# Kernel optimization log

Measured on AMD Instinct MI355X. Metric: run time of the kernel, lower is better.

Reference implementation:

```python
import jax, jax.numpy as jnp
import numpy as np

N = 10           # node count hardcoded in original module
FEAT_IN = 3      # position(2) + orientation(1)
FEAT_OUT = 16    # 'simple' mode
FEAT_CC = 2 * FEAT_OUT
B = 16384
NEG_SLOPE = 0.2


def _pair_index():
    # Faithful pair ordering: for node i, row 0 is the self-pair (i,i),
    # rows 1..N-1 are j != i in ascending order.
    idx = np.empty((N, N), dtype=np.int32)
    for i in range(N):
        idx[i, 0] = i
        idx[i, 1:] = [j for j in range(N) if j != i]
    return jnp.asarray(idx)


def setup_inputs() -> dict:
    key = jax.random.key(0)
    ks = jax.random.split(key, 12)
    s = 0.1
    return {
        "position": jax.random.normal(ks[0], (B, N, 2), dtype=jnp.float32),
        "orientation": jax.random.normal(ks[1], (B, N, 1), dtype=jnp.float32),
        # preliminary_transform: Linear(3 -> 16)
        "Wp": jax.random.normal(ks[2], (FEAT_IN, FEAT_OUT), dtype=jnp.float32) * s,
        "bp": jax.random.normal(ks[3], (FEAT_OUT,), dtype=jnp.float32) * s,
        # connectivity_net: Linear(32->32), LReLU, Linear(32->8), LReLU, Linear(8->2)
        "W1": jax.random.normal(ks[4], (FEAT_CC, 32), dtype=jnp.float32) * s,
        "b1": jax.random.normal(ks[5], (32,), dtype=jnp.float32) * s,
        "W2": jax.random.normal(ks[6], (32, 8), dtype=jnp.float32) * s,
        "b2": jax.random.normal(ks[7], (8,), dtype=jnp.float32) * s,
        "W3": jax.random.normal(ks[8], (8, 2), dtype=jnp.float32) * s,
        "b3": jax.random.normal(ks[9], (2,), dtype=jnp.float32) * s,
    }


def reference(position, orientation, Wp, bp, W1, b1, W2, b2, W3, b3):
    lrelu = lambda x: jnp.where(x >= 0, x, NEG_SLOPE * x)
    # [B, N, 3] -> [B, N, 16]
    feat = jnp.concatenate([position, orientation], axis=2) @ Wp + bp
    idx = _pair_index()                                   # [N, N]
    vj = feat[:, idx]                                     # [B, N, N, 16] gathered partners
    vi = jnp.broadcast_to(feat[:, :, None, :], vj.shape)  # [B, N, N, 16] source node
    pair = jnp.concatenate([vi, vj], axis=-1)             # [B, N, N, 32]
    h = lrelu(pair @ W1 + b1)
    h = lrelu(h @ W2 + b2)
    big_edge = h @ W3 + b3                                # [B, N, N, 2]
    adjacency = jnp.argmax(big_edge, axis=3)              # [B, N, N]
    return big_edge, adjacency
```

## Files before the change

kernel.cpp:

```cpp
#include <hip/hip_runtime.h>


typedef float v2f __attribute__((ext_vector_type(2)));
typedef float v4f __attribute__((ext_vector_type(4)));

constexpr int G = 12;
constexpr int GB_STRIDE = 36;
constexpr float NEG = 0.2f;

__global__ __launch_bounds__(256, 1) void fuse_kernel(
    const float* __restrict__ Wp, const float* __restrict__ bp,
    const float* __restrict__ W1, const float* __restrict__ b1,
    float* __restrict__ ws)
{
    const int t = threadIdx.x;
    if (t < 192) {
        const int d = t >> 6, k = t & 63;
        const int kk = k & 31;
        const int fo = (k < 32) ? 0 : 16;
        float acc = 0.f;
#pragma unroll
        for (int f = 0; f < 16; ++f)
            acc = fmaf(Wp[d * 16 + f], W1[(fo + f) * 32 + kk], acc);
        ws[d * 64 + k] = acc;
    } else {
        const int k = t - 192;
        const int kk = k & 31;
        const int fo = (k < 32) ? 0 : 16;
        float acc = 0.f;
#pragma unroll
        for (int f = 0; f < 16; ++f)
            acc = fmaf(bp[f], W1[(fo + f) * 32 + kk], acc);
        if (k < 32) acc += b1[k];
        ws[192 + k] = acc;
    }
}

__global__ __launch_bounds__(256, 4) void gpn_kernel(
    const float* __restrict__ pos,
    const float* __restrict__ ori,
    const float* __restrict__ ws,
    const float* __restrict__ W2,
    const float* __restrict__ b2,
    const float* __restrict__ W3,
    const float* __restrict__ b3,
    float* __restrict__ out,
    int B)
{
    __shared__ float sgb[G * 10 * GB_STRIDE];

    const int t = threadIdx.x;
    const int bBase = blockIdx.x * G;
    const int remG = B - bBase;
    const int nLanes = ((remG < G) ? remG : G) * 10 * 2;

    const v4f* m4 = (const v4f*)ws;
    const v4f* c4 = (const v4f*)(ws + 192);

    v4f ga[8];
    const int r = t >> 1;
    const int half = t & 1;
    const int g = r / 10;
    const int i = r - g * 10;
    if (t < nLanes) {
        const int node = bBase * 10 + r;
        const v2f p = ((const v2f*)pos)[node];
        const float o = ori[node];
        v4f* dst = (v4f*)&sgb[r * GB_STRIDE];
#pragma unroll
        for (int q = 0; q < 8; ++q) {
            v4f gg = c4[q];
            gg += p.x * m4[q];
            gg += p.y * m4[16 + q];
            gg += o   * m4[32 + q];
            ga[q] = gg;
        }
#pragma unroll
        for (int qq = 0; qq < 4; ++qq) {
            const int q = 8 + half * 4 + qq;
            v4f gg = c4[q];
            gg += p.x * m4[q];
            gg += p.y * m4[16 + q];
            gg += o   * m4[32 + q];
            dst[q - 8] = gg;
        }
    }
    __syncthreads();

    if (t < nLanes) {
        const v2f* w2p = (const v2f*)W2;
        const v2f* w3p = (const v2f*)W3;
        const v2f bb2_0 = ((const v2f*)b2)[0];
        const v2f bb2_1 = ((const v2f*)b2)[1];
        const v2f bb2_2 = ((const v2f*)b2)[2];
        const v2f bb2_3 = ((const v2f*)b2)[3];
        const v2f bb3   = ((const v2f*)b3)[0];

        const v4f* src[5];
#pragma unroll
        for (int e = 0; e < 5; ++e) {
            const int c = half * 5 + e;
            const int j = (c == 0) ? i : (((c - 1) < i) ? (c - 1) : c);
            src[e] = (const v4f*)&sgb[(g * 10 + j) * GB_STRIDE];
        }

        v2f A[5][4];
#pragma unroll
        for (int e = 0; e < 5; ++e) {
            A[e][0] = bb2_0; A[e][1] = bb2_1; A[e][2] = bb2_2; A[e][3] = bb2_3;
        }

#pragma unroll
        for (int q = 0; q < 8; ++q) {
            const v4f gaq = ga[q];
            const int k0 = 4 * q;
            const v2f w00 = w2p[4 * (k0 + 0) + 0], w01 = w2p[4 * (k0 + 0) + 1],
                      w02 = w2p[4 * (k0 + 0) + 2], w03 = w2p[4 * (k0 + 0) + 3];
            const v2f w10 = w2p[4 * (k0 + 1) + 0], w11 = w2p[4 * (k0 + 1) + 1],
                      w12 = w2p[4 * (k0 + 1) + 2], w13 = w2p[4 * (k0 + 1) + 3];
            const v2f w20 = w2p[4 * (k0 + 2) + 0], w21 = w2p[4 * (k0 + 2) + 1],
                      w22 = w2p[4 * (k0 + 2) + 2], w23 = w2p[4 * (k0 + 2) + 3];
            const v2f w30 = w2p[4 * (k0 + 3) + 0], w31 = w2p[4 * (k0 + 3) + 1],
                      w32 = w2p[4 * (k0 + 3) + 2], w33 = w2p[4 * (k0 + 3) + 3];
#pragma unroll
            for (int e = 0; e < 5; ++e) {
                const v4f s = gaq + src[e][q];
                const v4f h = __builtin_elementwise_max(s, s * NEG);
                A[e][0] += h.x * w00; A[e][1] += h.x * w01;
                A[e][2] += h.x * w02; A[e][3] += h.x * w03;
                A[e][0] += h.y * w10; A[e][1] += h.y * w11;
                A[e][2] += h.y * w12; A[e][3] += h.y * w13;
                A[e][0] += h.z * w20; A[e][1] += h.z * w21;
                A[e][2] += h.z * w22; A[e][3] += h.z * w23;
                A[e][0] += h.w * w30; A[e][1] += h.w * w31;
                A[e][2] += h.w * w32; A[e][3] += h.w * w33;
            }
        }

        const int eRow = (bBase + g) * 100 + i * 10;
        const size_t adjOff = (size_t)B * 200;
#pragma unroll
        for (int e = 0; e < 5; ++e) {
            const v2f h20 = __builtin_elementwise_max(A[e][0], A[e][0] * NEG);
            const v2f h21 = __builtin_elementwise_max(A[e][1], A[e][1] * NEG);
            const v2f h22 = __builtin_elementwise_max(A[e][2], A[e][2] * NEG);
            const v2f h23 = __builtin_elementwise_max(A[e][3], A[e][3] * NEG);

            v2f ev = bb3;
            ev += h20.x * w3p[0];
            ev += h20.y * w3p[1];
            ev += h21.x * w3p[2];
            ev += h21.y * w3p[3];
            ev += h22.x * w3p[4];
            ev += h22.y * w3p[5];
            ev += h23.x * w3p[6];
            ev += h23.y * w3p[7];

            const int E = eRow + half * 5 + e;
            ((v2f*)out)[E] = ev;
            out[adjOff + E] = (ev.y > ev.x) ? 1.0f : 0.0f;
        }
    }
}

extern "C" void kernel_launch(void* const* d_in, const int* in_sizes, int n_in,
                              void* d_out, int out_size, void* d_ws, size_t ws_size,
                              hipStream_t stream) {
    const float* pos = (const float*)d_in[0];
    const float* ori = (const float*)d_in[1];
    const float* Wp  = (const float*)d_in[2];
    const float* bp  = (const float*)d_in[3];
    const float* W1  = (const float*)d_in[4];
    const float* b1  = (const float*)d_in[5];
    const float* W2  = (const float*)d_in[6];
    const float* b2  = (const float*)d_in[7];
    const float* W3  = (const float*)d_in[8];
    const float* b3  = (const float*)d_in[9];
    float* out = (float*)d_out;
    float* ws  = (float*)d_ws;

    const int B = in_sizes[0] / 20;
    const int nBlocks = (B + G - 1) / G;

    fuse_kernel<<<1, 256, 0, stream>>>(Wp, bp, W1, b1, ws);
    gpn_kernel<<<nBlocks, 256, 0, stream>>>(pos, ori, ws, W2, b2, W3, b3, out, B);
}
```

Before: 95.17 us.

## Assign one thread per node row and vectorize output stores

Each thread now handles all 10 pairs of a node row instead of half of them. The block shrinks to 128 threads, and the thread count per row is halved. The per-node feature computation is no longer duplicated across two threads, and outputs are written as contiguous 16-byte and 8-byte vector stores instead of scattered 8-byte and 4-byte ones. In exchange, per-thread register use roughly doubles (ten accumulator sets), which lowers occupancy and halves total thread parallelism.

```diff
diff --git a/kernel.cpp b/kernel.cpp
--- a/kernel.cpp
+++ b/kernel.cpp
@@ -36,7 +36,7 @@
     }
 }
 
-__global__ __launch_bounds__(256, 4) void gpn_kernel(
+__global__ __launch_bounds__(128, 3) void gpn_kernel(
     const float* __restrict__ pos,
     const float* __restrict__ ori,
     const float* __restrict__ ws,
@@ -52,17 +52,16 @@
     const int t = threadIdx.x;
     const int bBase = blockIdx.x * G;
     const int remG = B - bBase;
-    const int nLanes = ((remG < G) ? remG : G) * 10 * 2;
+    const int nRows = ((remG < G) ? remG : G) * 10;
 
     const v4f* m4 = (const v4f*)ws;
     const v4f* c4 = (const v4f*)(ws + 192);
 
     v4f ga[8];
-    const int r = t >> 1;
-    const int half = t & 1;
+    const int r = t;
     const int g = r / 10;
     const int i = r - g * 10;
-    if (t < nLanes) {
+    if (r < nRows) {
         const int node = bBase * 10 + r;
         const v2f p = ((const v2f*)pos)[node];
         const float o = ori[node];
@@ -76,8 +75,7 @@
             ga[q] = gg;
         }
 #pragma unroll
-        for (int qq = 0; qq < 4; ++qq) {
-            const int q = 8 + half * 4 + qq;
+        for (int q = 8; q < 16; ++q) {
             v4f gg = c4[q];
             gg += p.x * m4[q];
             gg += p.y * m4[16 + q];
@@ -87,7 +85,7 @@
     }
     __syncthreads();
 
-    if (t < nLanes) {
+    if (r < nRows) {
         const v2f* w2p = (const v2f*)W2;
         const v2f* w3p = (const v2f*)W3;
         const v2f bb2_0 = ((const v2f*)b2)[0];
@@ -96,17 +94,16 @@
         const v2f bb2_3 = ((const v2f*)b2)[3];
         const v2f bb3   = ((const v2f*)b3)[0];
 
-        const v4f* src[5];
+        const v4f* src[10];
 #pragma unroll
-        for (int e = 0; e < 5; ++e) {
-            const int c = half * 5 + e;
+        for (int c = 0; c < 10; ++c) {
             const int j = (c == 0) ? i : (((c - 1) < i) ? (c - 1) : c);
-            src[e] = (const v4f*)&sgb[(g * 10 + j) * GB_STRIDE];
+            src[c] = (const v4f*)&sgb[(g * 10 + j) * GB_STRIDE];
         }
 
-        v2f A[5][4];
+        v2f A[10][4];
 #pragma unroll
-        for (int e = 0; e < 5; ++e) {
+        for (int e = 0; e < 10; ++e) {
             A[e][0] = bb2_0; A[e][1] = bb2_1; A[e][2] = bb2_2; A[e][3] = bb2_3;
         }
 
@@ -123,7 +120,7 @@
             const v2f w30 = w2p[4 * (k0 + 3) + 0], w31 = w2p[4 * (k0 + 3) + 1],
                       w32 = w2p[4 * (k0 + 3) + 2], w33 = w2p[4 * (k0 + 3) + 3];
 #pragma unroll
-            for (int e = 0; e < 5; ++e) {
+            for (int e = 0; e < 10; ++e) {
                 const v4f s = gaq + src[e][q];
                 const v4f h = __builtin_elementwise_max(s, s * NEG);
                 A[e][0] += h.x * w00; A[e][1] += h.x * w01;
@@ -137,10 +134,10 @@
             }
         }
 
-        const int eRow = (bBase + g) * 100 + i * 10;
-        const size_t adjOff = (size_t)B * 200;
+        float evb[20];
+        float adjv[10];
 #pragma unroll
-        for (int e = 0; e < 5; ++e) {
+        for (int e = 0; e < 10; ++e) {
             const v2f h20 = __builtin_elementwise_max(A[e][0], A[e][0] * NEG);
             const v2f h21 = __builtin_elementwise_max(A[e][1], A[e][1] * NEG);
             const v2f h22 = __builtin_elementwise_max(A[e][2], A[e][2] * NEG);
@@ -156,9 +153,23 @@
             ev += h23.x * w3p[6];
             ev += h23.y * w3p[7];
 
-            const int E = eRow + half * 5 + e;
-            ((v2f*)out)[E] = ev;
-            out[adjOff + E] = (ev.y > ev.x) ? 1.0f : 0.0f;
+            evb[2 * e]     = ev.x;
+            evb[2 * e + 1] = ev.y;
+            adjv[e] = (ev.y > ev.x) ? 1.0f : 0.0f;
+        }
+
+        const int eRow = (bBase + g) * 100 + i * 10;
+        v4f* bo = (v4f*)(out + (size_t)eRow * 2);
+#pragma unroll
+        for (int q = 0; q < 5; ++q) {
+            v4f vv = {evb[4 * q], evb[4 * q + 1], evb[4 * q + 2], evb[4 * q + 3]};
+            bo[q] = vv;
+        }
+        v2f* ao = (v2f*)(out + (size_t)B * 200 + eRow);
+#pragma unroll
+        for (int q = 0; q < 5; ++q) {
+            v2f vv = {adjv[2 * q], adjv[2 * q + 1]};
+            ao[q] = vv;
         }
     }
 }
@@ -183,5 +194,5 @@
     const int nBlocks = (B + G - 1) / G;
 
     fuse_kernel<<<1, 256, 0, stream>>>(Wp, bp, W1, b1, ws);
-    gpn_kernel<<<nBlocks, 256, 0, stream>>>(pos, ori, ws, W2, b2, W3, b3, out, B);
+    gpn_kernel<<<nBlocks, 128, 0, stream>>>(pos, ori, ws, W2, b2, W3, b3, out, B);
 }
```

Measured after the change: 94.86 us. No clear change (-0.3%).
